# Kernel optimization log

Hardware: AMD Instinct MI355X
Metric: run time of the kernel (lower is better)

## Reference

```python
import jax, jax.numpy as jnp
import numpy as np

B, C, H, W = 2, 1024, 64, 64
E, TOP_K = 8, 2
FFN = C  # ffn_dim = in_channels; hidden_dim = out_channels = in_channels


def setup_inputs() -> dict:
    key = jax.random.key(0)
    ks = jax.random.split(key, 5)
    s = 0.02
    return {
        "hidden_states": jax.random.normal(ks[0], (B, C, H, W), jnp.float32),
        "gate_w": jax.random.normal(ks[1], (E, C), jnp.float32) * s,   # torch Linear weight [out,in]
        "w1": jax.random.normal(ks[2], (E, FFN, C), jnp.float32) * s,
        "w2": jax.random.normal(ks[3], (E, C, FFN), jnp.float32) * s,
        "w3": jax.random.normal(ks[4], (E, FFN, C), jnp.float32) * s,
    }


def reference(hidden_states, gate_w, w1, w2, w3):
    b, c = hidden_states.shape[0], hidden_states.shape[1]
    space = hidden_states.shape[2:]
    # (B, C, H, W) -> (B, H, W, C) -> (T, C)
    x = jnp.transpose(hidden_states, (0, 2, 3, 1)).reshape(-1, c)

    # Router: softmax in float32, top-k, renormalize (matches torch)
    logits = x @ gate_w.T                                   # [T, E]
    probs = jax.nn.softmax(logits.astype(jnp.float32), axis=-1)
    rw, sel = jax.lax.top_k(probs, TOP_K)                   # [T, K]
    rw = rw / jnp.sum(rw, axis=-1, keepdims=True)
    rw = rw.astype(x.dtype)

    # Combine weights per expert: zero where expert not selected -> exact
    # equivalence with gather/scatter dispatch (full capacity, no drops).
    combine = jnp.sum(jax.nn.one_hot(sel, E, dtype=x.dtype) * rw[..., None], axis=1)  # [T, E]

    out = jnp.zeros_like(x)
    for e in range(E):  # small fixed expert loop
        h = jax.nn.gelu(x @ w1[e].T, approximate=False) * (x @ w3[e].T)  # SwiGLU-style [T, FFN]
        out = out + combine[:, e:e + 1] * (h @ w2[e].T)

    out = out.reshape(b, *space, c)
    return jnp.transpose(out, (0, 3, 1, 2))  # (B, C, H, W)
```

## Files before the change

### kernel.cpp

```cpp
#include <hip/hip_runtime.h>
#include <hip/hip_bf16.h>
#include <math.h>

#define BB 2
#define CC 1024
#define HH 64
#define WW 64
#define HWH (HH*WW)
#define TT (BB*HWH)
#define EE 8
#define FFN 1024
#define HCAP 17408
#define MAXTILES 136

typedef __bf16 bf16x8 __attribute__((ext_vector_type(8)));
typedef __bf16 bf16x4 __attribute__((ext_vector_type(4)));
typedef float  f32x4  __attribute__((ext_vector_type(4)));

__device__ __forceinline__ void gl_lds16(const __bf16* g, __bf16* l) {
    __builtin_amdgcn_global_load_lds(
        (const __attribute__((address_space(1))) void*)g,
        (__attribute__((address_space(3))) void*)l, 16, 0, 0);
}

__device__ __forceinline__ void barrier_raw() {
    asm volatile("" ::: "memory");
    __builtin_amdgcn_s_barrier();
    asm volatile("" ::: "memory");
}

#define CVB 12288
#define XPB 8192
#define RTB 512
__global__ __launch_bounds__(256) void k_prep(
    const float* __restrict__ hs, const float* __restrict__ gate_w,
    const float* __restrict__ w1, const float* __restrict__ w2,
    const float* __restrict__ w3,
    __bf16* __restrict__ w1b, __bf16* __restrict__ w2b,
    __bf16* __restrict__ w3b, __bf16* __restrict__ X,
    float* __restrict__ logP) {
    __shared__ float sm[2112];
    const int bid = blockIdx.x;
    const int tid = threadIdx.x;

    if (bid < CVB) {
        const float* s; __bf16* d; int lb = bid;
        if (lb < 4096)      { s = w1; d = w1b; }
        else if (lb < 8192) { s = w2; d = w2b; lb -= 4096; }
        else                { s = w3; d = w3b; lb -= 8192; }
        const size_t i = (size_t)lb * 2048 + (size_t)tid * 8;
        const f32x4 v0 = *(const f32x4*)&s[i];
        const f32x4 v1 = *(const f32x4*)&s[i + 4];
        bf16x8 o;
#pragma unroll
        for (int j = 0; j < 4; ++j) { o[j] = (__bf16)v0[j]; o[4 + j] = (__bf16)v1[j]; }
        *(bf16x8*)&d[i] = o;
    } else if (bid < CVB + XPB) {
        const int lb  = bid - CVB;
        const int hw0 = (lb & 127) * 32;
        const int c0  = ((lb >> 7) & 31) * 32;
        const int b   = lb >> 12;
        float (*tile)[33] = (float(*)[33])sm;
        const int tx = tid & 31, ty = tid >> 5;
        const float* src = hs + ((size_t)b * CC + c0) * HWH + hw0;
#pragma unroll
        for (int i = 0; i < 4; ++i)
            tile[ty + i * 8][tx] = src[(size_t)(ty + i * 8) * HWH + tx];
        __syncthreads();
        __bf16* dst = X + ((size_t)b * HWH + hw0) * CC + c0;
#pragma unroll
        for (int i = 0; i < 4; ++i) {
            const int hwl = ty + i * 8;
            dst[(size_t)hwl * CC + tx] = (__bf16)tile[tx][hwl];
        }
    } else {
        const int lb  = bid - (CVB + XPB);
        const int q   = lb & 3;
        const int t64 = lb >> 2;
        float* g = sm;
        for (int i = tid; i < 2048; i += 256)
            g[i] = gate_w[(size_t)(i >> 8) * CC + q * 256 + (i & 255)];
        __syncthreads();
        const int q2 = tid >> 6, tl = tid & 63;
        const int t  = t64 * 64 + tl;
        const int b  = t >> 12, hw = t & 4095;
        const float* xp = hs + (size_t)b * CC * HWH + hw;
        float l[EE];
#pragma unroll
        for (int e = 0; e < EE; ++e) l[e] = 0.0f;
        const int cbase = q * 256 + q2 * 64;
        for (int c2 = 0; c2 < 64; ++c2) {
            const float xv = xp[(size_t)(cbase + c2) * HWH];
#pragma unroll
            for (int e = 0; e < EE; ++e) l[e] += xv * g[e * 256 + q2 * 64 + c2];
        }
        float* dst = logP + ((size_t)(q * 4 + q2) * TT + t) * 8;
        f32x4 a, c;
#pragma unroll
        for (int e = 0; e < 4; ++e) { a[e] = l[e]; c[e] = l[4 + e]; }
        *(f32x4*)dst = a;
        *(f32x4*)&dst[4] = c;
    }
}

__global__ __launch_bounds__(256) void k_top2(const float* __restrict__ logP,
                                              int* __restrict__ cnt,
                                              int* __restrict__ idxl,
                                              int* __restrict__ tokE,
                                              int* __restrict__ tokP,
                                              float* __restrict__ tokW) {
    __shared__ int lcnt[EE], lbase[EE];
    const int tid = threadIdx.x;
    const int t   = blockIdx.x * 256 + tid;
    if (tid < EE) lcnt[tid] = 0;
    __syncthreads();

    float l[EE];
#pragma unroll
    for (int e = 0; e < EE; ++e) l[e] = 0.0f;
#pragma unroll
    for (int pq = 0; pq < 16; ++pq) {
        const float* src = logP + ((size_t)pq * TT + t) * 8;
        const f32x4 a = *(const f32x4*)src;
        const f32x4 c = *(const f32x4*)&src[4];
#pragma unroll
        for (int e = 0; e < 4; ++e) { l[e] += a[e]; l[4 + e] += c[e]; }
    }

    int e1 = 0; float v1 = l[0];
#pragma unroll
    for (int e = 1; e < EE; ++e) { if (l[e] > v1) { v1 = l[e]; e1 = e; } }
    int e2 = -1; float v2 = -1e30f;
#pragma unroll
    for (int e = 0; e < EE; ++e) { if (e != e1 && l[e] > v2) { v2 = l[e]; e2 = e; } }

    const float p2 = __expf(v2 - v1);
    const float rs = 1.0f / (1.0f + p2);

    const int m1 = atomicAdd(&lcnt[e1], 1);
    const int m2 = atomicAdd(&lcnt[e2], 1);
    __syncthreads();
    if (tid < EE) lbase[tid] = atomicAdd(&cnt[tid], lcnt[tid]);
    __syncthreads();
    const int p1pos = lbase[e1] + m1;
    const int p2pos = lbase[e2] + m2;

    idxl[e1 * TT + p1pos] = t;
    idxl[e2 * TT + p2pos] = t;
    tokE[t] = e1 | (e2 << 8);
    tokP[2 * t]     = p1pos;
    tokP[2 * t + 1] = p2pos;
    tokW[2 * t]     = rs;
    tokW[2 * t + 1] = p2 * rs;
}

__global__ void k_offsets(const int* __restrict__ cnt, int* __restrict__ off,
                          int* __restrict__ tileE, int* __restrict__ tileM,
                          int* __restrict__ nT) {
    if (threadIdx.x == 0) {
        int a = 0, n = 0;
        for (int e = 0; e < EE; ++e) {
            off[e] = a;
            const int mt = (cnt[e] + 127) >> 7;
            for (int m = 0; m < mt; ++m) { tileE[n] = e; tileM[n] = m * 128; ++n; }
            a += mt * 128;
        }
        nT[0] = n;
    }
}

__global__ __launch_bounds__(256, 2)
void k_gemm1(const __bf16* __restrict__ X, const __bf16* __restrict__ w1b,
             const __bf16* __restrict__ w3b, const int* __restrict__ cnt,
             const int* __restrict__ off, const int* __restrict__ idxl,
             const int* __restrict__ tileE, const int* __restrict__ tileM,
             const int* __restrict__ nT, __bf16* __restrict__ H) {
    if ((int)blockIdx.y >= nT[0]) return;
    const int e     = tileE[blockIdx.y];
    const int mt128 = tileM[blockIdx.y];
    const int cntE  = cnt[e];
    const int goff  = off[e];
    const int n0    = blockIdx.x * 128;
    const __bf16* W1 = w1b + (size_t)e * FFN * CC;
    const __bf16* W3 = w3b + (size_t)e * FFN * CC;

    __shared__ __bf16 sA[2][128 * 32];
    __shared__ __bf16 sB1[2][128 * 32];
    __shared__ __bf16 sB3[2][128 * 32];

    const int tid  = threadIdx.x;
    const int lane = tid & 63;
    const int wave = tid >> 6;
    const int wm   = (wave & 1) * 64;
    const int wn   = (wave >> 1) * 64;
    const int l15  = lane & 15;
    const int lq   = lane >> 4;
    const int rl   = lane >> 2;
    const int cpos = lane & 3;
    const int c8s = (cpos ^ ((rl >> 1) & 3)) * 8;
    const int cq  = ((lq ^ ((l15 >> 1) & 3))) * 8;

    int p0 = mt128 + wave * 32 + rl;      if (p0 > cntE - 1) p0 = cntE - 1;
    int p1 = mt128 + wave * 32 + 16 + rl; if (p1 > cntE - 1) p1 = cntE - 1;
    const __bf16* ga0  = X + (size_t)idxl[e * TT + p0] * CC + c8s;
    const __bf16* ga1  = X + (size_t)idxl[e * TT + p1] * CC + c8s;
    const __bf16* gb10 = W1 + (size_t)(n0 + wave * 32 + rl) * CC + c8s;
    const __bf16* gb11 = W1 + (size_t)(n0 + wave * 32 + 16 + rl) * CC + c8s;
    const __bf16* gb30 = W3 + (size_t)(n0 + wave * 32 + rl) * CC + c8s;
    const __bf16* gb31 = W3 + (size_t)(n0 + wave * 32 + 16 + rl) * CC + c8s;
    const int lofs0 = (wave * 32) * 32;
    const int lofs1 = (wave * 32 + 16) * 32;

    f32x4 acc1[4][4] = {};
    f32x4 acc3[4][4] = {};

    auto stage = [&](int b, int kb) {
        gl_lds16(ga0 + kb,  &sA[b][lofs0]);
        gl_lds16(ga1 + kb,  &sA[b][lofs1]);
        gl_lds16(gb10 + kb, &sB1[b][lofs0]);
        gl_lds16(gb11 + kb, &sB1[b][lofs1]);
        gl_lds16(gb30 + kb, &sB3[b][lofs0]);
        gl_lds16(gb31 + kb, &sB3[b][lofs1]);
    };

    stage(0, 0);
    int p = 0;
    for (int kb = 0; kb < CC; kb += 32, p ^= 1) {
        if (kb + 32 < CC) {
            stage(p ^ 1, kb + 32);
            asm volatile("s_waitcnt vmcnt(6)" ::: "memory");
        } else {
            asm volatile("s_waitcnt vmcnt(0)" ::: "memory");
        }
        barrier_raw();

        bf16x8 af[4], b1f[4], b3f[4];
#pragma unroll
        for (int i = 0; i < 4; ++i)
            af[i] = *(const bf16x8*)&sA[p][(wm + i * 16 + l15) * 32 + cq];
#pragma unroll
        for (int j = 0; j < 4; ++j)
            b1f[j] = *(const bf16x8*)&sB1[p][(wn + j * 16 + l15) * 32 + cq];
#pragma unroll
        for (int j = 0; j < 4; ++j)
            b3f[j] = *(const bf16x8*)&sB3[p][(wn + j * 16 + l15) * 32 + cq];
        asm volatile("s_waitcnt lgkmcnt(0)" ::: "memory");
        barrier_raw();

#pragma unroll
        for (int i = 0; i < 4; ++i)
#pragma unroll
            for (int j = 0; j < 4; ++j) {
                acc1[i][j] = __builtin_amdgcn_mfma_f32_16x16x32_bf16(
                    af[i], b1f[j], acc1[i][j], 0, 0, 0);
                acc3[i][j] = __builtin_amdgcn_mfma_f32_16x16x32_bf16(
                    af[i], b3f[j], acc3[i][j], 0, 0, 0);
            }
    }

#pragma unroll
    for (int i = 0; i < 4; ++i) {
        const int gb = goff + mt128 + wm + i * 16 + lq * 4;
#pragma unroll
        for (int j = 0; j < 4; ++j) {
            const int nb = n0 + wn + j * 16 + l15;
#pragma unroll
            for (int r = 0; r < 4; ++r) {
                const float a  = acc1[i][j][r];
                const float c  = acc3[i][j][r];
                const float ge = 0.5f * a * (1.0f + erff(a * 0.70710678118654752f));
                H[(size_t)(gb + r) * FFN + nb] = (__bf16)(ge * c);
            }
        }
    }
}

__global__ __launch_bounds__(256, 2)
void k_gemm2(const __bf16* __restrict__ H, const __bf16* __restrict__ w2b,
             const int* __restrict__ off, const int* __restrict__ tileE,
             const int* __restrict__ tileM, const int* __restrict__ nT,
             __bf16* __restrict__ Z) {
    if ((int)blockIdx.y >= nT[0]) return;
    const int e     = tileE[blockIdx.y];
    const int mt128 = tileM[blockIdx.y];
    const int goff  = off[e];
    const int n0    = blockIdx.x * 128;
    const __bf16* W2 = w2b + (size_t)e * CC * FFN;
    const __bf16* Arows = H + (size_t)(goff + mt128) * FFN;

    __shared__ __bf16 sA[2][128 * 32];
    __shared__ __bf16 sB[2][128 * 32];

    const int tid  = threadIdx.x;
    const int lane = tid & 63;
    const int wave = tid >> 6;
    const int wm   = (wave & 1) * 64;
    const int wn   = (wave >> 1) * 64;
    const int l15  = lane & 15;
    const int lq   = lane >> 4;
    const int rl   = lane >> 2;
    const int cpos = lane & 3;
    const int c8s = (cpos ^ ((rl >> 1) & 3)) * 8;
    const int cq  = ((lq ^ ((l15 >> 1) & 3))) * 8;

    const __bf16* ga0 = Arows + (size_t)(wave * 32 + rl) * FFN + c8s;
    const __bf16* ga1 = Arows + (size_t)(wave * 32 + 16 + rl) * FFN + c8s;
    const __bf16* gb0 = W2 + (size_t)(n0 + wave * 32 + rl) * FFN + c8s;
    const __bf16* gb1 = W2 + (size_t)(n0 + wave * 32 + 16 + rl) * FFN + c8s;
    const int lofs0 = (wave * 32) * 32;
    const int lofs1 = (wave * 32 + 16) * 32;

    f32x4 acc[4][4] = {};

    auto stage = [&](int b, int kb) {
        gl_lds16(ga0 + kb, &sA[b][lofs0]);
        gl_lds16(ga1 + kb, &sA[b][lofs1]);
        gl_lds16(gb0 + kb, &sB[b][lofs0]);
        gl_lds16(gb1 + kb, &sB[b][lofs1]);
    };

    stage(0, 0);
    int p = 0;
    for (int kb = 0; kb < FFN; kb += 32, p ^= 1) {
        if (kb + 32 < FFN) {
            stage(p ^ 1, kb + 32);
            asm volatile("s_waitcnt vmcnt(4)" ::: "memory");
        } else {
            asm volatile("s_waitcnt vmcnt(0)" ::: "memory");
        }
        barrier_raw();

        bf16x8 af[4], bf[4];
#pragma unroll
        for (int i = 0; i < 4; ++i)
            af[i] = *(const bf16x8*)&sA[p][(wm + i * 16 + l15) * 32 + cq];
#pragma unroll
        for (int j = 0; j < 4; ++j)
            bf[j] = *(const bf16x8*)&sB[p][(wn + j * 16 + l15) * 32 + cq];
        asm volatile("s_waitcnt lgkmcnt(0)" ::: "memory");
        barrier_raw();

#pragma unroll
        for (int i = 0; i < 4; ++i)
#pragma unroll
            for (int j = 0; j < 4; ++j)
                acc[i][j] = __builtin_amdgcn_mfma_f32_16x16x32_bf16(
                    af[i], bf[j], acc[i][j], 0, 0, 0);
    }

#pragma unroll
    for (int i = 0; i < 4; ++i) {
        const int gb = goff + mt128 + wm + i * 16 + lq * 4;
#pragma unroll
        for (int j = 0; j < 4; ++j) {
            const int c = n0 + wn + j * 16 + l15;
#pragma unroll
            for (int r = 0; r < 4; ++r)
                Z[(size_t)(gb + r) * CC + c] = (__bf16)acc[i][j][r];
        }
    }
}

__global__ __launch_bounds__(256) void k_combine(const __bf16* __restrict__ Z,
                                                 const int* __restrict__ off,
                                                 const int* __restrict__ tokE,
                                                 const int* __restrict__ tokP,
                                                 const float* __restrict__ tokW,
                                                 float* __restrict__ out) {
    __shared__ float tile[32][33];
    const int t0 = blockIdx.x * 32;
    const int c0 = blockIdx.y * 32;
    const int tx = threadIdx.x & 31;
    const int ty = threadIdx.x >> 5;

#pragma unroll
    for (int i = 0; i < 4; ++i) {
        const int tl = ty + 8 * i;
        const int t  = t0 + tl;
        const int ee = tokE[t];
        const int e1 = ee & 0xff, e2 = ee >> 8;
        const int r1 = off[e1] + tokP[2 * t];
        const int r2 = off[e2] + tokP[2 * t + 1];
        const float v = tokW[2 * t]     * (float)Z[(size_t)r1 * CC + c0 + tx]
                      + tokW[2 * t + 1] * (float)Z[(size_t)r2 * CC + c0 + tx];
        tile[tl][tx] = v;
    }
    __syncthreads();

    const int b   = t0 >> 12;
    const int hw0 = t0 & 4095;
#pragma unroll
    for (int i = 0; i < 4; ++i) {
        const int cl = ty + 8 * i;
        out[(size_t)b * CC * HWH + (size_t)(c0 + cl) * HWH + hw0 + tx] = tile[tx][cl];
    }
}

extern "C" void kernel_launch(void* const* d_in, const int* in_sizes, int n_in,
                              void* d_out, int out_size, void* d_ws, size_t ws_size,
                              hipStream_t stream) {
    const float* hs     = (const float*)d_in[0];
    const float* gate_w = (const float*)d_in[1];
    const float* w1     = (const float*)d_in[2];
    const float* w2     = (const float*)d_in[3];
    const float* w3     = (const float*)d_in[4];
    float* out = (float*)d_out;

    const size_t WSZ = (size_t)EE * FFN * CC * 2;
    char* ws = (char*)d_ws;
    __bf16* w2b  = (__bf16*)ws;
    __bf16* w1b  = (__bf16*)(ws + WSZ);
    __bf16* w3b  = (__bf16*)(ws + 2 * WSZ);
    __bf16* X    = (__bf16*)(ws + 3 * WSZ);
    __bf16* Zbuf = (__bf16*)(ws + WSZ);
    __bf16* Hbuf = (__bf16*)(ws + 4 * WSZ);
    float*  logP = (float*)Hbuf;
    char* p = ws + 4 * WSZ + (size_t)HCAP * FFN * 2;
    int*   idxl  = (int*)p;           p += (size_t)EE * TT * 4;
    int*   tokE  = (int*)p;           p += (size_t)TT * 4;
    int*   tokP  = (int*)p;           p += (size_t)2 * TT * 4;
    float* tokW  = (float*)p;         p += (size_t)2 * TT * 4;
    int*   cnt   = (int*)p;           p += 256;
    int*   off   = (int*)p;           p += 256;
    int*   tileE = (int*)p;           p += MAXTILES * 4;
    int*   tileM = (int*)p;           p += MAXTILES * 4;
    int*   nT    = (int*)p;

    hipMemsetAsync(cnt, 0, EE * sizeof(int), stream);

    k_prep<<<CVB + XPB + RTB, 256, 0, stream>>>(
        hs, gate_w, w1, w2, w3, w1b, w2b, w3b, X, logP);
    k_top2<<<TT / 256, 256, 0, stream>>>(logP, cnt, idxl, tokE, tokP, tokW);
    k_offsets<<<1, 64, 0, stream>>>(cnt, off, tileE, tileM, nT);

    k_gemm1<<<dim3(FFN / 128, MAXTILES), 256, 0, stream>>>(
        X, w1b, w3b, cnt, off, idxl, tileE, tileM, nT, Hbuf);
    k_gemm2<<<dim3(CC / 128, MAXTILES), 256, 0, stream>>>(
        Hbuf, w2b, off, tileE, tileM, nT, Zbuf);
    k_combine<<<dim3(TT / 32, CC / 32), 256, 0, stream>>>(
        Zbuf, off, tokE, tokP, tokW, out);
}
```

Measured before the change: 375.5 us.

## Enlarge grouped GEMM tiles to 256 rows with 4-stage LDS pipeline and 8 waves

Both expert GEMMs move to 512-thread blocks with 256-row M tiles, and gemm2 also uses 256-column N tiles. The double-buffered LDS staging becomes a 4-deep prefetch ring with interleaved half-tile MFMA phases, s_setprio, and explicit vmcnt waits. The loop is unrolled by hand. This aims to raise data reuse per block and hide global-to-LDS latency. The cost is more padding waste per expert from 256-row rounding, higher LDS use per block, and possible loss of occupancy.

Measured after the change: 383.5 us. 1.02x slower.

```diff
diff --git a/kernel.cpp b/kernel.cpp
--- a/kernel.cpp
+++ b/kernel.cpp
@@ -10,8 +10,8 @@
 #define TT (BB*HWH)
 #define EE 8
 #define FFN 1024
-#define HCAP 17408
-#define MAXTILES 136
+#define MAXTILES 71
+#define HCAP (MAXTILES*256)
 
 typedef __bf16 bf16x8 __attribute__((ext_vector_type(8)));
 typedef __bf16 bf16x4 __attribute__((ext_vector_type(4)));
@@ -28,6 +28,15 @@
     __builtin_amdgcn_s_barrier();
     asm volatile("" ::: "memory");
 }
+
+#define WAITV(N) asm volatile("s_waitcnt vmcnt(" #N ")" ::: "memory")
+#define LGKM0()  asm volatile("s_waitcnt lgkmcnt(0)" ::: "memory")
+
+#define MFMA16(ACC, AF, BF)                                                   \
+    _Pragma("unroll") for (int m_ = 0; m_ < 4; ++m_)                          \
+    _Pragma("unroll") for (int n_ = 0; n_ < 4; ++n_)                          \
+        ACC[m_][n_] = __builtin_amdgcn_mfma_f32_16x16x32_bf16(                \
+            AF[m_], BF[n_], ACC[m_][n_], 0, 0, 0);
 
 #define CVB 12288
 #define XPB 8192
@@ -161,113 +170,115 @@
         int a = 0, n = 0;
         for (int e = 0; e < EE; ++e) {
             off[e] = a;
-            const int mt = (cnt[e] + 127) >> 7;
-            for (int m = 0; m < mt; ++m) { tileE[n] = e; tileM[n] = m * 128; ++n; }
-            a += mt * 128;
+            const int mt = (cnt[e] + 255) >> 8;
+            for (int m = 0; m < mt; ++m) { tileE[n] = e; tileM[n] = m * 256; ++n; }
+            a += mt * 256;
         }
         nT[0] = n;
     }
 }
 
-__global__ __launch_bounds__(256, 2)
+__global__ __launch_bounds__(512, 2)
 void k_gemm1(const __bf16* __restrict__ X, const __bf16* __restrict__ w1b,
              const __bf16* __restrict__ w3b, const int* __restrict__ cnt,
              const int* __restrict__ off, const int* __restrict__ idxl,
              const int* __restrict__ tileE, const int* __restrict__ tileM,
              const int* __restrict__ nT, __bf16* __restrict__ H) {
     if ((int)blockIdx.y >= nT[0]) return;
-    const int e     = tileE[blockIdx.y];
-    const int mt128 = tileM[blockIdx.y];
-    const int cntE  = cnt[e];
-    const int goff  = off[e];
-    const int n0    = blockIdx.x * 128;
+    const int e    = tileE[blockIdx.y];
+    const int mt   = tileM[blockIdx.y];
+    const int cntE = cnt[e];
+    const int goff = off[e];
+    const int n0   = blockIdx.x * 128;
     const __bf16* W1 = w1b + (size_t)e * FFN * CC;
     const __bf16* W3 = w3b + (size_t)e * FFN * CC;
 
-    __shared__ __bf16 sA[2][128 * 32];
-    __shared__ __bf16 sB1[2][128 * 32];
-    __shared__ __bf16 sB3[2][128 * 32];
+    __shared__ __align__(16) __bf16 sA[4][256 * 32];
+    __shared__ __align__(16) __bf16 sB1[4][128 * 32];
+    __shared__ __align__(16) __bf16 sB3[4][128 * 32];
 
     const int tid  = threadIdx.x;
-    const int lane = tid & 63;
-    const int wave = tid >> 6;
-    const int wm   = (wave & 1) * 64;
-    const int wn   = (wave >> 1) * 64;
-    const int l15  = lane & 15;
-    const int lq   = lane >> 4;
-    const int rl   = lane >> 2;
-    const int cpos = lane & 3;
-    const int c8s = (cpos ^ ((rl >> 1) & 3)) * 8;
-    const int cq  = ((lq ^ ((l15 >> 1) & 3))) * 8;
-
-    int p0 = mt128 + wave * 32 + rl;      if (p0 > cntE - 1) p0 = cntE - 1;
-    int p1 = mt128 + wave * 32 + 16 + rl; if (p1 > cntE - 1) p1 = cntE - 1;
-    const __bf16* ga0  = X + (size_t)idxl[e * TT + p0] * CC + c8s;
-    const __bf16* ga1  = X + (size_t)idxl[e * TT + p1] * CC + c8s;
-    const __bf16* gb10 = W1 + (size_t)(n0 + wave * 32 + rl) * CC + c8s;
-    const __bf16* gb11 = W1 + (size_t)(n0 + wave * 32 + 16 + rl) * CC + c8s;
-    const __bf16* gb30 = W3 + (size_t)(n0 + wave * 32 + rl) * CC + c8s;
-    const __bf16* gb31 = W3 + (size_t)(n0 + wave * 32 + 16 + rl) * CC + c8s;
-    const int lofs0 = (wave * 32) * 32;
-    const int lofs1 = (wave * 32 + 16) * 32;
+    const int lane = tid & 63, wave = tid >> 6;
+    const int l15  = lane & 15, lq = (lane >> 4) & 3;
+    const int wm   = (wave >> 1) * 64;
+    const int wn   = (wave & 1) * 64;
+    const int cs   = (lq ^ (l15 & 3)) * 8;
+    const int r_l  = tid >> 2;
+    const int csw8 = ((tid & 3) ^ (r_l & 3)) * 8;
+
+    int p0 = mt + r_l;        if (p0 > cntE - 1) p0 = cntE - 1;
+    int p1 = mt + 128 + r_l;  if (p1 > cntE - 1) p1 = cntE - 1;
+    const __bf16* gA0 = X + (size_t)idxl[e * TT + p0] * CC + csw8;
+    const __bf16* gA1 = X + (size_t)idxl[e * TT + p1] * CC + csw8;
+    const __bf16* gW1 = W1 + (size_t)(n0 + r_l) * CC + csw8;
+    const __bf16* gW3 = W3 + (size_t)(n0 + r_l) * CC + csw8;
+
+    const int aoff = (wm + l15) * 32 + cs;
+    const int boff = (wn + l15) * 32 + cs;
+    const int dA   = wave * 512;
 
     f32x4 acc1[4][4] = {};
     f32x4 acc3[4][4] = {};
 
-    auto stage = [&](int b, int kb) {
-        gl_lds16(ga0 + kb,  &sA[b][lofs0]);
-        gl_lds16(ga1 + kb,  &sA[b][lofs1]);
-        gl_lds16(gb10 + kb, &sB1[b][lofs0]);
-        gl_lds16(gb11 + kb, &sB1[b][lofs1]);
-        gl_lds16(gb30 + kb, &sB3[b][lofs0]);
-        gl_lds16(gb31 + kb, &sB3[b][lofs1]);
-    };
-
-    stage(0, 0);
-    int p = 0;
-    for (int kb = 0; kb < CC; kb += 32, p ^= 1) {
-        if (kb + 32 < CC) {
-            stage(p ^ 1, kb + 32);
-            asm volatile("s_waitcnt vmcnt(6)" ::: "memory");
-        } else {
-            asm volatile("s_waitcnt vmcnt(0)" ::: "memory");
-        }
-        barrier_raw();
-
-        bf16x8 af[4], b1f[4], b3f[4];
-#pragma unroll
-        for (int i = 0; i < 4; ++i)
-            af[i] = *(const bf16x8*)&sA[p][(wm + i * 16 + l15) * 32 + cq];
-#pragma unroll
-        for (int j = 0; j < 4; ++j)
-            b1f[j] = *(const bf16x8*)&sB1[p][(wn + j * 16 + l15) * 32 + cq];
-#pragma unroll
-        for (int j = 0; j < 4; ++j)
-            b3f[j] = *(const bf16x8*)&sB3[p][(wn + j * 16 + l15) * 32 + cq];
-        asm volatile("s_waitcnt lgkmcnt(0)" ::: "memory");
-        barrier_raw();
-
-#pragma unroll
-        for (int i = 0; i < 4; ++i)
-#pragma unroll
-            for (int j = 0; j < 4; ++j) {
-                acc1[i][j] = __builtin_amdgcn_mfma_f32_16x16x32_bf16(
-                    af[i], b1f[j], acc1[i][j], 0, 0, 0);
-                acc3[i][j] = __builtin_amdgcn_mfma_f32_16x16x32_bf16(
-                    af[i], b3f[j], acc3[i][j], 0, 0, 0);
-            }
-    }
-
-#pragma unroll
-    for (int i = 0; i < 4; ++i) {
-        const int gb = goff + mt128 + wm + i * 16 + lq * 4;
-#pragma unroll
-        for (int j = 0; j < 4; ++j) {
-            const int nb = n0 + wn + j * 16 + l15;
+#define STG1A(S, KT) do { const int kb_ = (KT) * 32;                          \
+        gl_lds16(gA0 + kb_, &sA[S][dA]);                                      \
+        gl_lds16(gA1 + kb_, &sA[S][4096 + dA]); } while (0)
+#define STG1B(S, KT) do { const int kb_ = (KT) * 32;                          \
+        gl_lds16(gW1 + kb_, &sB1[S][dA]);                                     \
+        gl_lds16(gW3 + kb_, &sB3[S][dA]); } while (0)
+
+    STG1A(0, 0); STG1B(0, 0);
+    STG1A(1, 1); STG1B(1, 1);
+    STG1A(2, 2); STG1B(2, 2);
+    WAITV(8);
+    barrier_raw();
+
+#define TILE1(KT, S, PREF, WN) do {                                           \
+    bf16x8 af_[4], bf_[4];                                                    \
+    _Pragma("unroll") for (int i_ = 0; i_ < 4; ++i_) {                        \
+        af_[i_] = *(const bf16x8*)&sA[S][aoff + i_ * 512];                    \
+        bf_[i_] = *(const bf16x8*)&sB1[S][boff + i_ * 512];                   \
+    }                                                                         \
+    if (PREF) STG1A((S + 3) & 3, (KT) + 3);                                   \
+    barrier_raw();                                                            \
+    LGKM0();                                                                  \
+    __builtin_amdgcn_s_setprio(1);                                            \
+    MFMA16(acc1, af_, bf_);                                                   \
+    __builtin_amdgcn_s_setprio(0);                                            \
+    barrier_raw();                                                            \
+    _Pragma("unroll") for (int i_ = 0; i_ < 4; ++i_)                          \
+        bf_[i_] = *(const bf16x8*)&sB3[S][boff + i_ * 512];                   \
+    if (PREF) STG1B((S + 3) & 3, (KT) + 3);                                   \
+    barrier_raw();                                                            \
+    LGKM0();                                                                  \
+    __builtin_amdgcn_s_setprio(1);                                            \
+    MFMA16(acc3, af_, bf_);                                                   \
+    __builtin_amdgcn_s_setprio(0);                                            \
+    WAITV(WN);                                                                \
+    barrier_raw();                                                            \
+} while (0)
+
+    for (int k4 = 0; k4 < 28; k4 += 4) {
+        TILE1(k4 + 0, 0, 1, 8);
+        TILE1(k4 + 1, 1, 1, 8);
+        TILE1(k4 + 2, 2, 1, 8);
+        TILE1(k4 + 3, 3, 1, 8);
+    }
+    TILE1(28, 0, 1, 8);
+    TILE1(29, 1, 0, 4);
+    TILE1(30, 2, 0, 0);
+    TILE1(31, 3, 0, 63);
+
+#pragma unroll
+    for (int m = 0; m < 4; ++m) {
+        const int gb = goff + mt + wm + m * 16 + lq * 4;
+#pragma unroll
+        for (int n = 0; n < 4; ++n) {
+            const int nb = n0 + wn + n * 16 + l15;
 #pragma unroll
             for (int r = 0; r < 4; ++r) {
-                const float a  = acc1[i][j][r];
-                const float c  = acc3[i][j][r];
+                const float a  = acc1[m][n][r];
+                const float c  = acc3[m][n][r];
                 const float ge = 0.5f * a * (1.0f + erff(a * 0.70710678118654752f));
                 H[(size_t)(gb + r) * FFN + nb] = (__bf16)(ge * c);
             }
@@ -275,88 +286,104 @@
     }
 }
 
-__global__ __launch_bounds__(256, 2)
+__global__ __launch_bounds__(512, 2)
 void k_gemm2(const __bf16* __restrict__ H, const __bf16* __restrict__ w2b,
              const int* __restrict__ off, const int* __restrict__ tileE,
              const int* __restrict__ tileM, const int* __restrict__ nT,
              __bf16* __restrict__ Z) {
     if ((int)blockIdx.y >= nT[0]) return;
-    const int e     = tileE[blockIdx.y];
-    const int mt128 = tileM[blockIdx.y];
-    const int goff  = off[e];
-    const int n0    = blockIdx.x * 128;
+    const int e    = tileE[blockIdx.y];
+    const int mt   = tileM[blockIdx.y];
+    const int goff = off[e];
+    const int n0   = blockIdx.x * 256;
     const __bf16* W2 = w2b + (size_t)e * CC * FFN;
-    const __bf16* Arows = H + (size_t)(goff + mt128) * FFN;
-
-    __shared__ __bf16 sA[2][128 * 32];
-    __shared__ __bf16 sB[2][128 * 32];
+    const __bf16* Ar = H + (size_t)(goff + mt) * FFN;
+
+    __shared__ __align__(16) __bf16 sA[4][256 * 32];
+    __shared__ __align__(16) __bf16 sB[4][256 * 32];
 
     const int tid  = threadIdx.x;
-    const int lane = tid & 63;
-    const int wave = tid >> 6;
-    const int wm   = (wave & 1) * 64;
+    const int lane = tid & 63, wave = tid >> 6;
+    const int l15  = lane & 15, lq = (lane >> 4) & 3;
+    const int wm   = (wave & 1) * 128;
     const int wn   = (wave >> 1) * 64;
-    const int l15  = lane & 15;
-    const int lq   = lane >> 4;
-    const int rl   = lane >> 2;
-    const int cpos = lane & 3;
-    const int c8s = (cpos ^ ((rl >> 1) & 3)) * 8;
-    const int cq  = ((lq ^ ((l15 >> 1) & 3))) * 8;
-
-    const __bf16* ga0 = Arows + (size_t)(wave * 32 + rl) * FFN + c8s;
-    const __bf16* ga1 = Arows + (size_t)(wave * 32 + 16 + rl) * FFN + c8s;
-    const __bf16* gb0 = W2 + (size_t)(n0 + wave * 32 + rl) * FFN + c8s;
-    const __bf16* gb1 = W2 + (size_t)(n0 + wave * 32 + 16 + rl) * FFN + c8s;
-    const int lofs0 = (wave * 32) * 32;
-    const int lofs1 = (wave * 32 + 16) * 32;
-
-    f32x4 acc[4][4] = {};
-
-    auto stage = [&](int b, int kb) {
-        gl_lds16(ga0 + kb, &sA[b][lofs0]);
-        gl_lds16(ga1 + kb, &sA[b][lofs1]);
-        gl_lds16(gb0 + kb, &sB[b][lofs0]);
-        gl_lds16(gb1 + kb, &sB[b][lofs1]);
-    };
-
-    stage(0, 0);
-    int p = 0;
-    for (int kb = 0; kb < FFN; kb += 32, p ^= 1) {
-        if (kb + 32 < FFN) {
-            stage(p ^ 1, kb + 32);
-            asm volatile("s_waitcnt vmcnt(4)" ::: "memory");
-        } else {
-            asm volatile("s_waitcnt vmcnt(0)" ::: "memory");
-        }
-        barrier_raw();
-
-        bf16x8 af[4], bf[4];
-#pragma unroll
-        for (int i = 0; i < 4; ++i)
-            af[i] = *(const bf16x8*)&sA[p][(wm + i * 16 + l15) * 32 + cq];
-#pragma unroll
-        for (int j = 0; j < 4; ++j)
-            bf[j] = *(const bf16x8*)&sB[p][(wn + j * 16 + l15) * 32 + cq];
-        asm volatile("s_waitcnt lgkmcnt(0)" ::: "memory");
-        barrier_raw();
-
-#pragma unroll
-        for (int i = 0; i < 4; ++i)
-#pragma unroll
-            for (int j = 0; j < 4; ++j)
-                acc[i][j] = __builtin_amdgcn_mfma_f32_16x16x32_bf16(
-                    af[i], bf[j], acc[i][j], 0, 0, 0);
-    }
-
-#pragma unroll
-    for (int i = 0; i < 4; ++i) {
-        const int gb = goff + mt128 + wm + i * 16 + lq * 4;
-#pragma unroll
-        for (int j = 0; j < 4; ++j) {
-            const int c = n0 + wn + j * 16 + l15;
-#pragma unroll
-            for (int r = 0; r < 4; ++r)
-                Z[(size_t)(gb + r) * CC + c] = (__bf16)acc[i][j][r];
+    const int cs   = (lq ^ (l15 & 3)) * 8;
+    const int r_l  = tid >> 2;
+    const int csw8 = ((tid & 3) ^ (r_l & 3)) * 8;
+
+    const __bf16* gA0 = Ar + (size_t)r_l * FFN + csw8;
+    const __bf16* gA1 = Ar + (size_t)(128 + r_l) * FFN + csw8;
+    const __bf16* gB0 = W2 + (size_t)(n0 + r_l) * FFN + csw8;
+    const __bf16* gB1 = W2 + (size_t)(n0 + 128 + r_l) * FFN + csw8;
+
+    const int aoff = (wm + l15) * 32 + cs;
+    const int boff = (wn + l15) * 32 + cs;
+    const int dA   = wave * 512;
+
+    f32x4 accL[4][4] = {};
+    f32x4 accH[4][4] = {};
+
+#define STG2A(S, KT) do { const int kb_ = (KT) * 32;                          \
+        gl_lds16(gA0 + kb_, &sA[S][dA]);                                      \
+        gl_lds16(gA1 + kb_, &sA[S][4096 + dA]); } while (0)
+#define STG2B(S, KT) do { const int kb_ = (KT) * 32;                          \
+        gl_lds16(gB0 + kb_, &sB[S][dA]);                                      \
+        gl_lds16(gB1 + kb_, &sB[S][4096 + dA]); } while (0)
+
+    STG2A(0, 0); STG2B(0, 0);
+    STG2A(1, 1); STG2B(1, 1);
+    STG2A(2, 2); STG2B(2, 2);
+    WAITV(8);
+    barrier_raw();
+
+#define TILE2(KT, S, PREF, WN) do {                                           \
+    bf16x8 af_[4], bf_[4];                                                    \
+    _Pragma("unroll") for (int i_ = 0; i_ < 4; ++i_) {                        \
+        af_[i_] = *(const bf16x8*)&sA[S][aoff + i_ * 512];                    \
+        bf_[i_] = *(const bf16x8*)&sB[S][boff + i_ * 512];                    \
+    }                                                                         \
+    if (PREF) STG2A((S + 3) & 3, (KT) + 3);                                   \
+    barrier_raw();                                                            \
+    LGKM0();                                                                  \
+    __builtin_amdgcn_s_setprio(1);                                            \
+    MFMA16(accL, af_, bf_);                                                   \
+    __builtin_amdgcn_s_setprio(0);                                            \
+    barrier_raw();                                                            \
+    _Pragma("unroll") for (int i_ = 0; i_ < 4; ++i_)                          \
+        af_[i_] = *(const bf16x8*)&sA[S][aoff + 2048 + i_ * 512];             \
+    if (PREF) STG2B((S + 3) & 3, (KT) + 3);                                   \
+    barrier_raw();                                                            \
+    LGKM0();                                                                  \
+    __builtin_amdgcn_s_setprio(1);                                            \
+    MFMA16(accH, af_, bf_);                                                   \
+    __builtin_amdgcn_s_setprio(0);                                            \
+    WAITV(WN);                                                                \
+    barrier_raw();                                                            \
+} while (0)
+
+    for (int k4 = 0; k4 < 28; k4 += 4) {
+        TILE2(k4 + 0, 0, 1, 8);
+        TILE2(k4 + 1, 1, 1, 8);
+        TILE2(k4 + 2, 2, 1, 8);
+        TILE2(k4 + 3, 3, 1, 8);
+    }
+    TILE2(28, 0, 1, 8);
+    TILE2(29, 1, 0, 4);
+    TILE2(30, 2, 0, 0);
+    TILE2(31, 3, 0, 63);
+
+#pragma unroll
+    for (int m = 0; m < 4; ++m) {
+#pragma unroll
+        for (int n = 0; n < 4; ++n) {
+            const int nb = n0 + wn + n * 16 + l15;
+#pragma unroll
+            for (int r = 0; r < 4; ++r) {
+                Z[(size_t)(goff + mt + wm + m * 16 + lq * 4 + r) * CC + nb] =
+                    (__bf16)accL[m][n][r];
+                Z[(size_t)(goff + mt + wm + 64 + m * 16 + lq * 4 + r) * CC + nb] =
+                    (__bf16)accH[m][n][r];
+            }
         }
     }
 }
@@ -433,9 +460,9 @@
     k_top2<<<TT / 256, 256, 0, stream>>>(logP, cnt, idxl, tokE, tokP, tokW);
     k_offsets<<<1, 64, 0, stream>>>(cnt, off, tileE, tileM, nT);
 
-    k_gemm1<<<dim3(FFN / 128, MAXTILES), 256, 0, stream>>>(
+    k_gemm1<<<dim3(FFN / 128, MAXTILES), 512, 0, stream>>>(
         X, w1b, w3b, cnt, off, idxl, tileE, tileM, nT, Hbuf);
-    k_gemm2<<<dim3(CC / 128, MAXTILES), 256, 0, stream>>>(
+    k_gemm2<<<dim3(CC / 256, MAXTILES), 512, 0, stream>>>(
         Hbuf, w2b, off, tileE, tileM, nT, Zbuf);
     k_combine<<<dim3(TT / 32, CC / 32), 256, 0, stream>>>(
         Zbuf, off, tokE, tokP, tokW, out);
```
